# Performance work log

Measured on AMD Instinct MI355X. Metric: run time of the kernel, lower is better.

The kernel has to match this reference:

```python
import jax, jax.numpy as jnp
import numpy as np

N_LEVELS = 16
LOG2_T = 19
T = 1 << LOG2_T
BASE = 16
MAXRES = 4096
F = 2
MAXC = 16  # (max_SH_degree+1)^2
PER_LEVEL_SCALE = float(np.exp((np.log(MAXRES) - np.log(BASE)) / (N_LEVELS - 1)))
RES = jnp.asarray([BASE * PER_LEVEL_SCALE ** l for l in range(N_LEVELS)], dtype=jnp.float32)
PRIMES = jnp.array([1, 2654435761, 805459861], dtype=jnp.uint32)
OFFS = jnp.asarray([[(i >> 2) & 1, (i >> 1) & 1, i & 1] for i in range(8)], dtype=jnp.int32)  # (8,3)

C0 = 0.28209479177387814
C1 = 0.4886025119029199
C2 = (1.0925484305920792, -1.0925484305920792, 0.31539156525252005, -1.0925484305920792, 0.5462742152960396)
C3 = (-0.5900435899266435, 2.890611442640554, -0.4570457994644658, 0.3731763325901154, -0.4570457994644658, 1.445305721320277, -0.5900435899266435)


def hash_encode(x, table):
    # x: (N,3) in [0,1]; table: (L,T,F). Multiresolution hash grid (tcnn HashGrid).
    def level(tab, res):
        p = x * res
        p0 = jnp.floor(p)
        w = p - p0                                  # (N,3) trilerp weights
        c = p0.astype(jnp.uint32)[:, None, :] + OFFS[None].astype(jnp.uint32)  # (N,8,3)
        h = (c[..., 0] * PRIMES[0]) ^ (c[..., 1] * PRIMES[1]) ^ (c[..., 2] * PRIMES[2])
        idx = (h & jnp.uint32(T - 1)).astype(jnp.int32)
        f = tab[idx]                                # (N,8,F) irregular gather
        wc = jnp.where(OFFS[None].astype(bool), w[:, None, :], 1.0 - w[:, None, :]).prod(-1)
        return (f * wc[..., None]).sum(1)           # (N,F)
    feats = jax.vmap(level)(table, RES)             # (L,N,F)
    return feats.transpose(1, 0, 2).reshape(x.shape[0], N_LEVELS * F)


def sh_basis(d):
    # real SH basis up to degree 3; d: (N,3) unit vectors -> (N,16)
    x, y, z = d[..., 0], d[..., 1], d[..., 2]
    xx, yy, zz = x * x, y * y, z * z
    xy, yz, xz = x * y, y * z, x * z
    return jnp.stack([
        jnp.full_like(x, C0), -C1 * y, C1 * z, -C1 * x,
        C2[0] * xy, C2[1] * yz, C2[2] * (2 * zz - xx - yy), C2[3] * xz, C2[4] * (xx - yy),
        C3[0] * y * (3 * xx - yy), C3[1] * xy * z, C3[2] * y * (4 * zz - xx - yy),
        C3[3] * z * (2 * zz - 3 * xx - 3 * yy), C3[4] * x * (4 * zz - xx - yy),
        C3[5] * z * (xx - yy), C3[6] * x * (xx - 3 * yy)], axis=-1)


def network_forward(positions, rx_pos, table, W1, W2, aabb, active_deg):
    aabb_min, aabb_max = aabb[:3], aabb[3:]
    scale = jnp.maximum(aabb_max - aabb_min, 1e-6)
    norm_pos = (positions - aabb_min) / scale
    selector = jnp.all((norm_pos >= 0.0) & (norm_pos <= 1.0), axis=-1)  # (N,)
    pos_n = jnp.clip(norm_pos, 0.0, 1.0)  # safe values for masked-out points (zeroed below)

    def density_fn(pn):
        feats = hash_encode(pn, table)
        h = jax.nn.relu(feats @ W1)
        sh = (h @ W2).reshape(-1, MAXC, 2)
        dens = C0 * sh[:, 0, :]                     # (N,2) = (real, imag) of sigma
        return jnp.sqrt(dens[:, 0] ** 2 + dens[:, 1] ** 2).sum(), (dens, sh)

    # in-forward autograd: grad of sum |sigma| w.r.t. normalized positions
    (_, (dens, sh)), g = jax.value_and_grad(density_fn, has_aux=True)(pos_n)
    g_world = g / scale
    nrm = -g_world / jnp.maximum(jnp.linalg.norm(g_world, axis=-1, keepdims=True), 1e-20)
    nrm = jnp.where(jnp.isnan(nrm), 0.0, nrm)

    # EvalSH: view direction from sample point toward receiver, SH dot coefficients
    dirs = rx_pos - positions
    dirs = dirs / jnp.maximum(jnp.linalg.norm(dirs, axis=-1, keepdims=True), 1e-20)
    Y = sh_basis(dirs)                              # (N,16)
    mask = (jnp.arange(MAXC) < (active_deg + 1) ** 2).astype(Y.dtype)
    scat = jnp.einsum('nc,ncf->nf', Y * mask, sh)   # (N,2) complex as (re,im)

    sel = selector[:, None]
    dens = jnp.where(sel, dens, 0.0)
    scat = jnp.where(sel, scat, 0.0)
    nrm = jnp.where(sel, nrm, 0.0)
    shz = jnp.where(selector[:, None, None], sh, 0.0)
    # pack: sigma(re,im) | scatterers_to(re,im) | normals(3) | sh_coeffs(32) -> (N,39)
    return jnp.concatenate([dens, scat, nrm, shz.reshape(-1, MAXC * 2)], axis=-1)


def setup_inputs() -> dict:
    key = jax.random.key(0)
    ks = jax.random.split(key, 6)
    N = 262144
    positions = jax.random.uniform(ks[0], (N, 3), jnp.float32) * 2.2 - 1.1
    rx_pos = jax.random.normal(ks[1], (3,), jnp.float32) * 2.0
    table = (jax.random.uniform(ks[2], (N_LEVELS, T, F), jnp.float32) * 2.0 - 1.0) * 1e-4
    d_in, hid, d_out = N_LEVELS * F, 32, MAXC * 2
    W1 = jax.random.normal(ks[3], (d_in, hid), jnp.float32) / np.sqrt(d_in)
    W2 = jax.random.normal(ks[4], (hid, d_out), jnp.float32) / np.sqrt(hid)
    aabb = jnp.array([-1.0, -1.0, -1.0, 1.0, 1.0, 1.0], jnp.float32)
    return {"positions": positions, "rx_pos": rx_pos, "table": table, "W1": W1,
            "W2": W2, "aabb": aabb, "active_deg": 3}


def reference(positions, rx_pos, table, W1, W2, aabb, active_deg):
    return network_forward(positions, rx_pos, table, W1, W2, aabb, active_deg)
```

## Files before the change

kernel.cpp:

```cpp
#include <hip/hip_runtime.h>
#include <cmath>

#pragma clang fp contract(off)

#define NLV 16
#define TSZ (1u << 19)
#define TMASK (TSZ - 1u)
#define PR1 2654435761u
#define PR2 805459861u

struct ResT { float r[NLV]; };

__device__ __forceinline__ void aabb_norm(
    const float* __restrict__ g_aabb, float posx, float posy, float posz,
    float& s0, float& s1, float& s2,
    float& pnx, float& pny, float& pnz, bool& sel)
{
    float a0 = g_aabb[0], a1 = g_aabb[1], a2 = g_aabb[2];
    s0 = fmaxf(g_aabb[3] - a0, 1e-6f);
    s1 = fmaxf(g_aabb[4] - a1, 1e-6f);
    s2 = fmaxf(g_aabb[5] - a2, 1e-6f);
    float nx = (posx - a0) / s0;
    float ny = (posy - a1) / s1;
    float nz = (posz - a2) / s2;
    sel = (nx >= 0.f) && (nx <= 1.f) && (ny >= 0.f) && (ny <= 1.f)
       && (nz >= 0.f) && (nz <= 1.f);
    pnx = fminf(fmaxf(nx, 0.f), 1.f);
    pny = fminf(fmaxf(ny, 0.f), 1.f);
    pnz = fminf(fmaxf(nz, 0.f), 1.f);
}

__global__ __launch_bounds__(256) void level_gather(
    const float* __restrict__ g_pos,
    const float* __restrict__ g_tab,
    const float* __restrict__ g_aabb,
    float* __restrict__ ws,
    int N, ResT rt)
{
    int b = blockIdx.x;
    int lvl = b & 15;
    int n = (b >> 4) * 256 + threadIdx.x;
    if (n >= N) return;

    float posx = g_pos[3*n+0], posy = g_pos[3*n+1], posz = g_pos[3*n+2];
    float s0, s1, s2, pnx, pny, pnz; bool sel;
    aabb_norm(g_aabb, posx, posy, posz, s0, s1, s2, pnx, pny, pnz, sel);

    float res = rt.r[lvl];
    const float2* tl = (const float2*)g_tab + (size_t)lvl * TSZ;

    float fx = pnx * res, fy = pny * res, fz = pnz * res;
    float x0 = floorf(fx), y0 = floorf(fy), z0 = floorf(fz);
    float wx = fx - x0, wy = fy - y0, wz = fz - z0;
    float omx = 1.f - wx, omy = 1.f - wy, omz = 1.f - wz;
    unsigned ux = (unsigned)x0, uy = (unsigned)y0, uz = (unsigned)z0;
    unsigned hx0 = ux,        hx1 = ux + 1u;
    unsigned hy0 = uy * PR1,  hy1 = (uy + 1u) * PR1;
    unsigned hz0 = uz * PR2,  hz1 = (uz + 1u) * PR2;
    float f0 = 0.f, f1 = 0.f;
    float lxa = 0.f, lxb = 0.f, lya = 0.f, lyb = 0.f, lza = 0.f, lzb = 0.f;
#pragma unroll
    for (int c = 0; c < 8; ++c) {
        unsigned hh = ((c & 4) ? hx1 : hx0) ^ ((c & 2) ? hy1 : hy0) ^ ((c & 1) ? hz1 : hz0);
        float2 fv = tl[hh & TMASK];
        float wxv = (c & 4) ? wx : omx;
        float wyv = (c & 2) ? wy : omy;
        float wzv = (c & 1) ? wz : omz;
        float wgt = wxv * wyv;
        wgt = wgt * wzv;
        float t0 = fv.x * wgt;
        float t1 = fv.y * wgt;
        f0 = f0 + t0;
        f1 = f1 + t1;
        float pyz = wyv * wzv;
        float pxz = wxv * wzv;
        float pxy = wxv * wyv;
        float spx = (c & 4) ? pyz : -pyz;
        float spy = (c & 2) ? pxz : -pxz;
        float spz = (c & 1) ? pxy : -pxy;
        lxa = lxa + fv.x * spx;  lxb = lxb + fv.y * spx;
        lya = lya + fv.x * spy;  lyb = lyb + fv.y * spy;
        lza = lza + fv.x * spz;  lzb = lzb + fv.y * spz;
    }

    size_t LN = (size_t)NLV * N;
    size_t base = (size_t)lvl * N + n;
    ws[0*LN + base] = f0;
    ws[1*LN + base] = f1;
    ws[2*LN + base] = lxa;
    ws[3*LN + base] = lxb;
    ws[4*LN + base] = lya;
    ws[5*LN + base] = lyb;
    ws[6*LN + base] = lza;
    ws[7*LN + base] = lzb;
}

__global__ __launch_bounds__(256) void mlp_bwd(
    const float* __restrict__ g_pos,
    const float* __restrict__ g_rx,
    const float* __restrict__ g_W1,
    const float* __restrict__ g_W2,
    const float* __restrict__ g_aabb,
    const int*   __restrict__ g_deg,
    const float* __restrict__ ws,
    float* __restrict__ g_out,
    int N, ResT rt)
{
    int n = blockIdx.x * 256 + threadIdx.x;
    if (n >= N) return;

    float posx = g_pos[3*n+0], posy = g_pos[3*n+1], posz = g_pos[3*n+2];
    float s0, s1, s2, pnx, pny, pnz; bool sel;
    aabb_norm(g_aabb, posx, posy, posz, s0, s1, s2, pnx, pny, pnz, sel);
    (void)pnx; (void)pny; (void)pnz;

    size_t LN = (size_t)NLV * N;
    const float* f0w = ws + 0*LN;
    const float* f1w = ws + 1*LN;

    float z1[32];
#pragma unroll
    for (int i = 0; i < 32; ++i) z1[i] = 0.f;
    for (int l = 0; l < NLV; ++l) {
        float f0 = f0w[(size_t)l * N + n];
        float f1 = f1w[(size_t)l * N + n];
        const float* w1a = g_W1 + (2*l) * 32;
        const float* w1b = g_W1 + (2*l+1) * 32;
#pragma unroll
        for (int i = 0; i < 32; ++i) {
            float acc = fmaf(f0, w1a[i], z1[i]);
            z1[i] = fmaf(f1, w1b[i], acc);
        }
    }

    unsigned mask = 0u;
    float sh[32];
#pragma unroll
    for (int o = 0; o < 32; ++o) sh[o] = 0.f;
#pragma unroll
    for (int i = 0; i < 32; ++i) {
        bool on = (z1[i] > 0.f);
        if (on) mask |= (1u << i);
        float h = on ? z1[i] : 0.f;
        const float* w2r = g_W2 + i * 32;
#pragma unroll
        for (int o = 0; o < 32; ++o) sh[o] = fmaf(h, w2r[o], sh[o]);
    }

    const float C0c = 0.28209479177387814f;
    float d0 = C0c * sh[0], d1 = C0c * sh[1];

    float rx0 = g_rx[0], rx1 = g_rx[1], rx2 = g_rx[2];
    float dxw = rx0 - posx, dyw = rx1 - posy, dzw = rx2 - posz;
    float dnorm = sqrtf(dxw*dxw + dyw*dyw + dzw*dzw);
    float dinv = 1.f / fmaxf(dnorm, 1e-20f);
    float X = dxw * dinv, Yd = dyw * dinv, Z = dzw * dinv;
    float xx = X*X, yy = Yd*Yd, zz = Z*Z;
    float xy = X*Yd, yz = Yd*Z, xz = X*Z;
    float Yb[16];
    Yb[0]  = 0.28209479177387814f;
    Yb[1]  = -0.4886025119029199f * Yd;
    Yb[2]  =  0.4886025119029199f * Z;
    Yb[3]  = -0.4886025119029199f * X;
    Yb[4]  =  1.0925484305920792f * xy;
    Yb[5]  = -1.0925484305920792f * yz;
    Yb[6]  =  0.31539156525252005f * (2.f*zz - xx - yy);
    Yb[7]  = -1.0925484305920792f * xz;
    Yb[8]  =  0.5462742152960396f * (xx - yy);
    Yb[9]  = -0.5900435899266435f * Yd * (3.f*xx - yy);
    Yb[10] =  2.890611442640554f  * xy * Z;
    Yb[11] = -0.4570457994644658f * Yd * (4.f*zz - xx - yy);
    Yb[12] =  0.3731763325901154f * Z * (2.f*zz - 3.f*xx - 3.f*yy);
    Yb[13] = -0.4570457994644658f * X * (4.f*zz - xx - yy);
    Yb[14] =  1.445305721320277f  * Z * (xx - yy);
    Yb[15] = -0.5900435899266435f * X * (xx - 3.f*yy);

    int deg = g_deg[0];
    int nact = (deg + 1) * (deg + 1);
    float sc0 = 0.f, sc1 = 0.f;
#pragma unroll
    for (int c = 0; c < 16; ++c) {
        float yc = (c < nact) ? Yb[c] : 0.f;
        sc0 = fmaf(yc, sh[2*c+0], sc0);
        sc1 = fmaf(yc, sh[2*c+1], sc1);
    }

    float* op = g_out + (size_t)n * 39;
    op[0] = sel ? d0  : 0.f;
    op[1] = sel ? d1  : 0.f;
    op[2] = sel ? sc0 : 0.f;
    op[3] = sel ? sc1 : 0.f;
#pragma unroll
    for (int c = 0; c < 32; ++c) op[7 + c] = sel ? sh[c] : 0.f;

    float ss = d0*d0 + d1*d1;
    float q0 = 0.f, q1 = 0.f;
    if (ss > 0.f) {
        float sr = sqrtf(ss);
        q0 = C0c * d0 / sr;
        q1 = C0c * d1 / sr;
    }
    float dzv[32];
#pragma unroll
    for (int i = 0; i < 32; ++i) {
        float dh = fmaf(q0, g_W2[i*32+0], q1 * g_W2[i*32+1]);
        dzv[i] = ((mask >> i) & 1u) ? dh : 0.f;
    }

    const float* mxaw = ws + 2*LN;
    const float* mxbw = ws + 3*LN;
    const float* myaw = ws + 4*LN;
    const float* mybw = ws + 5*LN;
    const float* mzaw = ws + 6*LN;
    const float* mzbw = ws + 7*LN;
    float gx = 0.f, gy = 0.f, gz = 0.f;
    const float4* w1v = (const float4*)g_W1;
    for (int l = 0; l < NLV; ++l) {
        const float4* wa = w1v + (size_t)(2*l) * 8;
        const float4* wb = wa + 8;
        float da = 0.f, db = 0.f;
#pragma unroll
        for (int k = 0; k < 8; ++k) {
            float4 va = wa[k], vb = wb[k];
            da = fmaf(va.x, dzv[4*k+0], da);
            da = fmaf(va.y, dzv[4*k+1], da);
            da = fmaf(va.z, dzv[4*k+2], da);
            da = fmaf(va.w, dzv[4*k+3], da);
            db = fmaf(vb.x, dzv[4*k+0], db);
            db = fmaf(vb.y, dzv[4*k+1], db);
            db = fmaf(vb.z, dzv[4*k+2], db);
            db = fmaf(vb.w, dzv[4*k+3], db);
        }
        size_t base = (size_t)l * N + n;
        float xa = mxaw[base], xb = mxbw[base];
        float ya = myaw[base], yb = mybw[base];
        float za = mzaw[base], zb = mzbw[base];
        float res = rt.r[l];
        gx = fmaf(res, fmaf(da, xa, db * xb), gx);
        gy = fmaf(res, fmaf(da, ya, db * yb), gy);
        gz = fmaf(res, fmaf(da, za, db * zb), gz);
    }

    float gwx = gx / s0, gwy = gy / s1, gwz = gz / s2;
    float gn = sqrtf(gwx*gwx + gwy*gwy + gwz*gwz);
    float ginv = -1.f / fmaxf(gn, 1e-20f);
    op[4] = sel ? gwx * ginv : 0.f;
    op[5] = sel ? gwy * ginv : 0.f;
    op[6] = sel ? gwz * ginv : 0.f;
}

__global__ __launch_bounds__(256, 2) void ngp_fused(
    const float* __restrict__ g_pos,
    const float* __restrict__ g_rx,
    const float* __restrict__ g_tab,
    const float* __restrict__ g_W1,
    const float* __restrict__ g_W2,
    const float* __restrict__ g_aabb,
    const int*   __restrict__ g_deg,
    float* __restrict__ g_out,
    int N, ResT rt)
{
    __shared__ float sm[48][256];

    int tid = blockIdx.x * 256 + threadIdx.x;
    int lt  = threadIdx.x;
    int n = tid >> 1;
    int p = tid & 1;
    if (n >= N) return;

    float posx = g_pos[3*n+0], posy = g_pos[3*n+1], posz = g_pos[3*n+2];
    float s0, s1, s2, pnx, pny, pnz; bool sel;
    aabb_norm(g_aabb, posx, posy, posz, s0, s1, s2, pnx, pny, pnz, sel);

    const float2* tab = (const float2*)g_tab;
    float f0o[8], f1o[8];
#pragma unroll
    for (int j = 0; j < 8; ++j) {
        float res = p ? rt.r[8+j] : rt.r[j];
        const float2* tl = tab + (size_t)(p * 8 + j) * TSZ;
        float fx = pnx * res, fy = pny * res, fz = pnz * res;
        float x0 = floorf(fx), y0 = floorf(fy), z0 = floorf(fz);
        float wx = fx - x0, wy = fy - y0, wz = fz - z0;
        float omx = 1.f - wx, omy = 1.f - wy, omz = 1.f - wz;
        unsigned ux = (unsigned)x0, uy = (unsigned)y0, uz = (unsigned)z0;
        unsigned hx0 = ux,        hx1 = ux + 1u;
        unsigned hy0 = uy * PR1,  hy1 = (uy + 1u) * PR1;
        unsigned hz0 = uz * PR2,  hz1 = (uz + 1u) * PR2;
        float f0 = 0.f, f1 = 0.f;
        float lxa = 0.f, lxb = 0.f, lya = 0.f, lyb = 0.f, lza = 0.f, lzb = 0.f;
#pragma unroll
        for (int c = 0; c < 8; ++c) {
            unsigned hh = ((c & 4) ? hx1 : hx0) ^ ((c & 2) ? hy1 : hy0) ^ ((c & 1) ? hz1 : hz0);
            float2 fv = tl[hh & TMASK];
            float wxv = (c & 4) ? wx : omx;
            float wyv = (c & 2) ? wy : omy;
            float wzv = (c & 1) ? wz : omz;
            float wgt = wxv * wyv;
            wgt = wgt * wzv;
            float t0 = fv.x * wgt;
            float t1 = fv.y * wgt;
            f0 = f0 + t0;
            f1 = f1 + t1;
            float pyz = wyv * wzv;
            float pxz = wxv * wzv;
            float pxy = wxv * wyv;
            float spx = (c & 4) ? pyz : -pyz;
            float spy = (c & 2) ? pxz : -pxz;
            float spz = (c & 1) ? pxy : -pxy;
            lxa = lxa + fv.x * spx;  lxb = lxb + fv.y * spx;
            lya = lya + fv.x * spy;  lyb = lyb + fv.y * spy;
            lza = lza + fv.x * spz;  lzb = lzb + fv.y * spz;
        }
        f0o[j] = f0; f1o[j] = f1;
        sm[j*6+0][lt] = lxa;  sm[j*6+1][lt] = lxb;
        sm[j*6+2][lt] = lya;  sm[j*6+3][lt] = lyb;
        sm[j*6+4][lt] = lza;  sm[j*6+5][lt] = lzb;
    }

    float z1[32];
#pragma unroll
    for (int i = 0; i < 32; ++i) z1[i] = 0.f;
    float hi0[8], hi1[8];
#pragma unroll
    for (int j = 0; j < 8; ++j) {
        float t0 = __shfl_xor(f0o[j], 1, 64);
        float t1 = __shfl_xor(f1o[j], 1, 64);
        float lo0 = p ? t0 : f0o[j];
        float lo1 = p ? t1 : f1o[j];
        hi0[j] = p ? f0o[j] : t0;
        hi1[j] = p ? f1o[j] : t1;
        const float* w1a = g_W1 + (2*j) * 32;
        const float* w1b = g_W1 + (2*j+1) * 32;
#pragma unroll
        for (int i = 0; i < 32; ++i) {
            float acc = fmaf(lo0, w1a[i], z1[i]);
            z1[i] = fmaf(lo1, w1b[i], acc);
        }
    }
#pragma unroll
    for (int j = 0; j < 8; ++j) {
        const float* w1a = g_W1 + (2*(8+j)) * 32;
        const float* w1b = g_W1 + (2*(8+j)+1) * 32;
#pragma unroll
        for (int i = 0; i < 32; ++i) {
            float acc = fmaf(hi0[j], w1a[i], z1[i]);
            z1[i] = fmaf(hi1[j], w1b[i], acc);
        }
    }

    unsigned mask = 0u;
    float sh[32];
#pragma unroll
    for (int o = 0; o < 32; ++o) sh[o] = 0.f;
#pragma unroll
    for (int i = 0; i < 32; ++i) {
        bool on = (z1[i] > 0.f);
        if (on) mask |= (1u << i);
        float h = on ? z1[i] : 0.f;
        const float* w2r = g_W2 + i * 32;
#pragma unroll
        for (int o = 0; o < 32; ++o) sh[o] = fmaf(h, w2r[o], sh[o]);
    }

    const float C0c = 0.28209479177387814f;
    float d0 = C0c * sh[0], d1 = C0c * sh[1];

    float rx0 = g_rx[0], rx1 = g_rx[1], rx2 = g_rx[2];
    float dxw = rx0 - posx, dyw = rx1 - posy, dzw = rx2 - posz;
    float dnorm = sqrtf(dxw*dxw + dyw*dyw + dzw*dzw);
    float dinv = 1.f / fmaxf(dnorm, 1e-20f);
    float X = dxw * dinv, Yd = dyw * dinv, Z = dzw * dinv;
    float xx = X*X, yy = Yd*Yd, zz = Z*Z;
    float xy = X*Yd, yz = Yd*Z, xz = X*Z;
    float Yb[16];
    Yb[0]  = 0.28209479177387814f;
    Yb[1]  = -0.4886025119029199f * Yd;
    Yb[2]  =  0.4886025119029199f * Z;
    Yb[3]  = -0.4886025119029199f * X;
    Yb[4]  =  1.0925484305920792f * xy;
    Yb[5]  = -1.0925484305920792f * yz;
    Yb[6]  =  0.31539156525252005f * (2.f*zz - xx - yy);
    Yb[7]  = -1.0925484305920792f * xz;
    Yb[8]  =  0.5462742152960396f * (xx - yy);
    Yb[9]  = -0.5900435899266435f * Yd * (3.f*xx - yy);
    Yb[10] =  2.890611442640554f  * xy * Z;
    Yb[11] = -0.4570457994644658f * Yd * (4.f*zz - xx - yy);
    Yb[12] =  0.3731763325901154f * Z * (2.f*zz - 3.f*xx - 3.f*yy);
    Yb[13] = -0.4570457994644658f * X * (4.f*zz - xx - yy);
    Yb[14] =  1.445305721320277f  * Z * (xx - yy);
    Yb[15] = -0.5900435899266435f * X * (xx - 3.f*yy);

    int deg = g_deg[0];
    int nact = (deg + 1) * (deg + 1);
    float sc0 = 0.f, sc1 = 0.f;
#pragma unroll
    for (int c = 0; c < 16; ++c) {
        float yc = (c < nact) ? Yb[c] : 0.f;
        sc0 = fmaf(yc, sh[2*c+0], sc0);
        sc1 = fmaf(yc, sh[2*c+1], sc1);
    }

    float* op = g_out + (size_t)n * 39;
    if (p == 0) {
        op[0] = sel ? d0  : 0.f;
        op[1] = sel ? d1  : 0.f;
        op[2] = sel ? sc0 : 0.f;
        op[3] = sel ? sc1 : 0.f;
#pragma unroll
        for (int c = 0; c < 13; ++c) op[7 + c] = sel ? sh[c] : 0.f;
    } else {
#pragma unroll
        for (int c = 13; c < 32; ++c) op[7 + c] = sel ? sh[c] : 0.f;
    }

    float ss = d0*d0 + d1*d1;
    float q0 = 0.f, q1 = 0.f;
    if (ss > 0.f) {
        float sr = sqrtf(ss);
        q0 = C0c * d0 / sr;
        q1 = C0c * d1 / sr;
    }
    float dzv[32];
#pragma unroll
    for (int i = 0; i < 32; ++i) {
        float dh = fmaf(q0, g_W2[i*32+0], q1 * g_W2[i*32+1]);
        dzv[i] = ((mask >> i) & 1u) ? dh : 0.f;
    }

    float gx = 0.f, gy = 0.f, gz = 0.f;
    const float4* w1v = (const float4*)g_W1;
    int rbase = p * 16;
#pragma unroll
    for (int j = 0; j < 8; ++j) {
        const float4* wa = w1v + (size_t)(rbase + 2*j) * 8;
        const float4* wb = wa + 8;
        float da = 0.f, db = 0.f;
#pragma unroll
        for (int k = 0; k < 8; ++k) {
            float4 va = wa[k], vb = wb[k];
            da = fmaf(va.x, dzv[4*k+0], da);
            da = fmaf(va.y, dzv[4*k+1], da);
            da = fmaf(va.z, dzv[4*k+2], da);
            da = fmaf(va.w, dzv[4*k+3], da);
            db = fmaf(vb.x, dzv[4*k+0], db);
            db = fmaf(vb.y, dzv[4*k+1], db);
            db = fmaf(vb.z, dzv[4*k+2], db);
            db = fmaf(vb.w, dzv[4*k+3], db);
        }
        float xa = sm[j*6+0][lt], xb = sm[j*6+1][lt];
        float ya = sm[j*6+2][lt], yb = sm[j*6+3][lt];
        float za = sm[j*6+4][lt], zb = sm[j*6+5][lt];
        float res = p ? rt.r[8+j] : rt.r[j];
        gx = fmaf(res, fmaf(da, xa, db * xb), gx);
        gy = fmaf(res, fmaf(da, ya, db * yb), gy);
        gz = fmaf(res, fmaf(da, za, db * zb), gz);
    }
    float tx = __shfl_xor(gx, 1, 64);
    float ty = __shfl_xor(gy, 1, 64);
    float tz = __shfl_xor(gz, 1, 64);
    gx = gx + tx; gy = gy + ty; gz = gz + tz;

    float gwx = gx / s0, gwy = gy / s1, gwz = gz / s2;
    float gn = sqrtf(gwx*gwx + gwy*gwy + gwz*gwz);
    float ginv = -1.f / fmaxf(gn, 1e-20f);
    if (p == 0) {
        op[4] = sel ? gwx * ginv : 0.f;
        op[5] = sel ? gwy * ginv : 0.f;
        op[6] = sel ? gwz * ginv : 0.f;
    }
}

extern "C" void kernel_launch(void* const* d_in, const int* in_sizes, int n_in,
                              void* d_out, int out_size, void* d_ws, size_t ws_size,
                              hipStream_t stream)
{
    const float* g_pos  = (const float*)d_in[0];
    const float* g_rx   = (const float*)d_in[1];
    const float* g_tab  = (const float*)d_in[2];
    const float* g_W1   = (const float*)d_in[3];
    const float* g_W2   = (const float*)d_in[4];
    const float* g_aabb = (const float*)d_in[5];
    const int*   g_deg  = (const int*)d_in[6];
    float* g_out = (float*)d_out;

    int N = in_sizes[0] / 3;

    ResT rt;
    double scale = exp((log(4096.0) - log(16.0)) / 15.0);
    for (int l = 0; l < NLV; ++l) rt.r[l] = (float)(16.0 * pow(scale, (double)l));

    size_t need = (size_t)NLV * N * 8 * sizeof(float);
    if (ws_size >= need) {
        float* ws = (float*)d_ws;
        int chunks = (N + 255) / 256;
        level_gather<<<NLV * chunks, 256, 0, stream>>>(g_pos, g_tab, g_aabb,
                                                       ws, N, rt);
        mlp_bwd<<<chunks, 256, 0, stream>>>(g_pos, g_rx, g_W1, g_W2, g_aabb,
                                            g_deg, ws, g_out, N, rt);
    } else {
        long long threads = 2LL * N;
        int blocks = (int)((threads + 255) / 256);
        ngp_fused<<<blocks, 256, 0, stream>>>(g_pos, g_rx, g_tab, g_W1, g_W2,
                                              g_aabb, g_deg, g_out, N, rt);
    }
}
```

Baseline: 357.7 us.

## Vectorize workspace layout, add nontemporal stores, and split level scheduling in halves

The per-level workspace moves from eight scalar planes to interleaved vector planes (float2 features, float4 x/y partials, float2 z partials). Both kernels now write and read these with single vector nontemporal accesses and prefetch the next level. The gather kernel's block-to-level mapping is changed so that the first half of the grid covers levels 0-7 and the second half covers levels 8-15, which keeps table accesses more local in time. Output stores are made nontemporal as well. The aim is fewer memory transactions and less cache pollution, at the cost of more registers in mlp_bwd from the full unroll and the preloaded features.

```diff
diff --git a/kernel.cpp b/kernel.cpp
--- a/kernel.cpp
+++ b/kernel.cpp
@@ -8,6 +8,9 @@
 #define TMASK (TSZ - 1u)
 #define PR1 2654435761u
 #define PR2 805459861u
+
+typedef float v2f __attribute__((ext_vector_type(2)));
+typedef float v4f __attribute__((ext_vector_type(4)));
 
 struct ResT { float r[NLV]; };
 
@@ -35,11 +38,13 @@
     const float* __restrict__ g_tab,
     const float* __restrict__ g_aabb,
     float* __restrict__ ws,
-    int N, ResT rt)
+    int N, int chunks, ResT rt)
 {
     int b = blockIdx.x;
-    int lvl = b & 15;
-    int n = (b >> 4) * 256 + threadIdx.x;
+    int half = (b >= 8 * chunks) ? 1 : 0;
+    int bb = b - half * (8 * chunks);
+    int lvl = (bb & 7) + (half << 3);
+    int n = (bb >> 3) * 256 + threadIdx.x;
     if (n >= N) return;
 
     float posx = g_pos[3*n+0], posy = g_pos[3*n+1], posz = g_pos[3*n+2];
@@ -84,15 +89,16 @@
     }
 
     size_t LN = (size_t)NLV * N;
-    size_t base = (size_t)lvl * N + n;
-    ws[0*LN + base] = f0;
-    ws[1*LN + base] = f1;
-    ws[2*LN + base] = lxa;
-    ws[3*LN + base] = lxb;
-    ws[4*LN + base] = lya;
-    ws[5*LN + base] = lyb;
-    ws[6*LN + base] = lza;
-    ws[7*LN + base] = lzb;
+    size_t idx = (size_t)lvl * N + n;
+    v2f* f2 = (v2f*)ws;
+    v4f* p4 = (v4f*)(ws + 2*LN);
+    v2f* p2 = (v2f*)(ws + 6*LN);
+    v2f ff = {f0, f1};
+    v4f pa = {lxa, lxb, lya, lyb};
+    v2f pz = {lza, lzb};
+    __builtin_nontemporal_store(ff, f2 + idx);
+    __builtin_nontemporal_store(pa, p4 + idx);
+    __builtin_nontemporal_store(pz, p2 + idx);
 }
 
 __global__ __launch_bounds__(256) void mlp_bwd(
@@ -115,15 +121,22 @@
     (void)pnx; (void)pny; (void)pnz;
 
     size_t LN = (size_t)NLV * N;
-    const float* f0w = ws + 0*LN;
-    const float* f1w = ws + 1*LN;
+    const v2f* f2 = (const v2f*)ws;
+    const v4f* p4 = (const v4f*)(ws + 2*LN);
+    const v2f* p2 = (const v2f*)(ws + 6*LN);
+
+    v2f fv[NLV];
+#pragma unroll
+    for (int l = 0; l < NLV; ++l)
+        fv[l] = __builtin_nontemporal_load(f2 + (size_t)l * N + n);
 
     float z1[32];
 #pragma unroll
     for (int i = 0; i < 32; ++i) z1[i] = 0.f;
+#pragma unroll
     for (int l = 0; l < NLV; ++l) {
-        float f0 = f0w[(size_t)l * N + n];
-        float f1 = f1w[(size_t)l * N + n];
+        float f0 = fv[l].x;
+        float f1 = fv[l].y;
         const float* w1a = g_W1 + (2*l) * 32;
         const float* w1b = g_W1 + (2*l+1) * 32;
 #pragma unroll
@@ -186,12 +199,13 @@
     }
 
     float* op = g_out + (size_t)n * 39;
-    op[0] = sel ? d0  : 0.f;
-    op[1] = sel ? d1  : 0.f;
-    op[2] = sel ? sc0 : 0.f;
-    op[3] = sel ? sc1 : 0.f;
-#pragma unroll
-    for (int c = 0; c < 32; ++c) op[7 + c] = sel ? sh[c] : 0.f;
+    __builtin_nontemporal_store(sel ? d0  : 0.f, op + 0);
+    __builtin_nontemporal_store(sel ? d1  : 0.f, op + 1);
+    __builtin_nontemporal_store(sel ? sc0 : 0.f, op + 2);
+    __builtin_nontemporal_store(sel ? sc1 : 0.f, op + 3);
+#pragma unroll
+    for (int c = 0; c < 32; ++c)
+        __builtin_nontemporal_store(sel ? sh[c] : 0.f, op + 7 + c);
 
     float ss = d0*d0 + d1*d1;
     float q0 = 0.f, q1 = 0.f;
@@ -207,15 +221,17 @@
         dzv[i] = ((mask >> i) & 1u) ? dh : 0.f;
     }
 
-    const float* mxaw = ws + 2*LN;
-    const float* mxbw = ws + 3*LN;
-    const float* myaw = ws + 4*LN;
-    const float* mybw = ws + 5*LN;
-    const float* mzaw = ws + 6*LN;
-    const float* mzbw = ws + 7*LN;
+    v4f c4 = __builtin_nontemporal_load(p4 + n);
+    v2f c2 = __builtin_nontemporal_load(p2 + n);
     float gx = 0.f, gy = 0.f, gz = 0.f;
     const float4* w1v = (const float4*)g_W1;
+#pragma unroll
     for (int l = 0; l < NLV; ++l) {
+        v4f n4 = c4; v2f n2 = c2;
+        if (l + 1 < NLV) {
+            n4 = __builtin_nontemporal_load(p4 + (size_t)(l+1) * N + n);
+            n2 = __builtin_nontemporal_load(p2 + (size_t)(l+1) * N + n);
+        }
         const float4* wa = w1v + (size_t)(2*l) * 8;
         const float4* wb = wa + 8;
         float da = 0.f, db = 0.f;
@@ -231,22 +247,19 @@
             db = fmaf(vb.z, dzv[4*k+2], db);
             db = fmaf(vb.w, dzv[4*k+3], db);
         }
-        size_t base = (size_t)l * N + n;
-        float xa = mxaw[base], xb = mxbw[base];
-        float ya = myaw[base], yb = mybw[base];
-        float za = mzaw[base], zb = mzbw[base];
         float res = rt.r[l];
-        gx = fmaf(res, fmaf(da, xa, db * xb), gx);
-        gy = fmaf(res, fmaf(da, ya, db * yb), gy);
-        gz = fmaf(res, fmaf(da, za, db * zb), gz);
+        gx = fmaf(res, fmaf(da, c4.x, db * c4.y), gx);
+        gy = fmaf(res, fmaf(da, c4.z, db * c4.w), gy);
+        gz = fmaf(res, fmaf(da, c2.x, db * c2.y), gz);
+        c4 = n4; c2 = n2;
     }
 
     float gwx = gx / s0, gwy = gy / s1, gwz = gz / s2;
     float gn = sqrtf(gwx*gwx + gwy*gwy + gwz*gwz);
     float ginv = -1.f / fmaxf(gn, 1e-20f);
-    op[4] = sel ? gwx * ginv : 0.f;
-    op[5] = sel ? gwy * ginv : 0.f;
-    op[6] = sel ? gwz * ginv : 0.f;
+    __builtin_nontemporal_store(sel ? gwx * ginv : 0.f, op + 4);
+    __builtin_nontemporal_store(sel ? gwy * ginv : 0.f, op + 5);
+    __builtin_nontemporal_store(sel ? gwz * ginv : 0.f, op + 6);
 }
 
 __global__ __launch_bounds__(256, 2) void ngp_fused(
@@ -494,7 +507,7 @@
         float* ws = (float*)d_ws;
         int chunks = (N + 255) / 256;
         level_gather<<<NLV * chunks, 256, 0, stream>>>(g_pos, g_tab, g_aabb,
-                                                       ws, N, rt);
+                                                       ws, N, chunks, rt);
         mlp_bwd<<<chunks, 256, 0, stream>>>(g_pos, g_rx, g_W1, g_W2, g_aabb,
                                             g_deg, ws, g_out, N, rt);
     } else {
```

Measured after the change: 393.2 us. 1.1x slower.
